# Kernel optimization log

Hardware: AMD Instinct MI355X
Metric: run time of the kernel (lower is better)

The kernel has to match this reference:

```python
import jax, jax.numpy as jnp
import numpy as np

NUM_HEADS = 16
HEAD_DIM = 80
DIM = NUM_HEADS * HEAD_DIM
SEQ = 2048
SCALE = HEAD_DIM ** -0.5


def rotate_half(x):
    x1, x2 = jnp.split(x, 2, axis=-1)
    return jnp.concatenate((-x2, x1), axis=-1)


def setup_inputs() -> dict:
    key = jax.random.key(0)
    ks = jax.random.split(key, 8)
    hidden_states = jax.random.normal(ks[0], (SEQ, DIM), dtype=jnp.float32)
    cu_seqlens = jnp.array([0, SEQ], dtype=jnp.int32)  # unused by the math
    # rotary embeddings for head_dim
    inv_freq = 1.0 / (10000.0 ** (jnp.arange(0, HEAD_DIM // 2, dtype=jnp.float32) / (HEAD_DIM // 2)))
    freqs = jnp.outer(jnp.arange(SEQ, dtype=jnp.float32), inv_freq)  # [S, hd/2]
    emb = jnp.concatenate((freqs, freqs), axis=-1)  # [S, hd]
    cos = jnp.cos(emb)
    sin = jnp.sin(emb)
    w_qkv = jax.random.normal(ks[1], (3 * DIM, DIM), dtype=jnp.float32) * (DIM ** -0.5)
    b_qkv = jax.random.normal(ks[2], (3 * DIM,), dtype=jnp.float32) * 0.02
    w_proj = jax.random.normal(ks[3], (DIM, DIM), dtype=jnp.float32) * (DIM ** -0.5)
    b_proj = jax.random.normal(ks[4], (DIM,), dtype=jnp.float32) * 0.02
    return {"hidden_states": hidden_states, "cu_seqlens": cu_seqlens, "cos": cos,
            "sin": sin, "w_qkv": w_qkv, "b_qkv": b_qkv, "w_proj": w_proj, "b_proj": b_proj}


def reference(hidden_states, cu_seqlens, cos, sin, w_qkv, b_qkv, w_proj, b_proj):
    S = hidden_states.shape[0]
    qkv = hidden_states @ w_qkv.T + b_qkv  # [S, 3*D]
    qkv = qkv.reshape(S, 3, NUM_HEADS, HEAD_DIM)
    q, k, v = qkv[:, 0], qkv[:, 1], qkv[:, 2]  # each [S, H, hd]
    c = cos[:, None, :]  # [S, 1, hd]
    s = sin[:, None, :]
    q = q * c + rotate_half(q) * s
    k = k * c + rotate_half(k) * s
    # SDPA, non-causal: [H, S, S]
    scores = jnp.einsum('shd,thd->hst', q, k) * SCALE
    attn = jax.nn.softmax(scores, axis=-1)
    out = jnp.einsum('hst,thd->shd', attn, v).reshape(S, DIM)
    return out @ w_proj.T + b_proj
```

## Files before the change

### kernel.cpp

```cpp
#include <hip/hip_runtime.h>


#define SEQLEN   2048
#define DIMM     1280
#define NHEADS   16
#define HD       80
#define HDP      96
#define QKV_N    3840
#define NSPLIT   4
#define KVSPAN   (SEQLEN / NSPLIT)
#define QSCALE_LOG2E 0.16130083587064776f

#define KSTRIDE  104
#define VSTRIDE  72

#define EXP2F(x) __builtin_amdgcn_exp2f(x)

#define GLD16(gptr, lptr)                                                      \
    __builtin_amdgcn_global_load_lds(                                          \
        (const __attribute__((address_space(1))) void*)(gptr),                 \
        (__attribute__((address_space(3))) void*)(lptr), 16, 0, 0)

typedef float f32x4 __attribute__((ext_vector_type(4)));
typedef _Float16 half8 __attribute__((ext_vector_type(8)));
typedef _Float16 half4 __attribute__((ext_vector_type(4)));

static __device__ __forceinline__ f32x4 mfma_16x16x32(half8 a, half8 b, f32x4 c) {
    return __builtin_amdgcn_mfma_f32_16x16x32_f16(a, b, c, 0, 0, 0);
}
static __device__ __forceinline__ f32x4 mfma_16x16x16(half4 a, half4 b, f32x4 c) {
    return __builtin_amdgcn_mfma_f32_16x16x16f16(a, b, c, 0, 0, 0);
}

__global__ __launch_bounds__(256)
void cast_all(const float* __restrict__ hs, const float* __restrict__ wq,
              const float* __restrict__ wp, _Float16* __restrict__ dhs,
              _Float16* __restrict__ dwq, _Float16* __restrict__ dwp) {
    const int n1 = SEQLEN * DIMM / 4, n2 = QKV_N * DIMM / 4, n3 = DIMM * DIMM / 4;
    int i = blockIdx.x * 256 + threadIdx.x;
    const float4* src; half4* dst; int j;
    if (i < n1)           { src = (const float4*)hs; dst = (half4*)dhs; j = i; }
    else if (i < n1 + n2) { src = (const float4*)wq; dst = (half4*)dwq; j = i - n1; }
    else if (i < n1 + n2 + n3) { src = (const float4*)wp; dst = (half4*)dwp; j = i - n1 - n2; }
    else return;
    const float4 v = src[j];
    half4 h;
    h.x = (_Float16)v.x; h.y = (_Float16)v.y;
    h.z = (_Float16)v.z; h.w = (_Float16)v.w;
    dst[j] = h;
}

template<bool OUT_F16>
__global__ __launch_bounds__(256, 2)
void gemm_bt(const _Float16* __restrict__ A, const _Float16* __restrict__ B,
             const float* __restrict__ bias, void* __restrict__ Cout,
             int M, int N, int K) {
    __shared__ __align__(16) _Float16 As[128 * 32];
    __shared__ __align__(16) _Float16 Bs[128 * 32];
    const int tid  = threadIdx.x;
    const int lane = tid & 63;
    const int wave = tid >> 6;
    const int l15  = lane & 15;
    const int quad = lane >> 4;
    const int wm   = wave & 1;
    const int wn   = wave >> 1;
    const long bm = blockIdx.x, bn = blockIdx.y;

    const _Float16* Ag = A + bm * 128 * (long)K;
    const _Float16* Bg = B + bn * 128 * (long)K;

    const int srow = lane >> 2;
    const int scol = (lane & 3) * 8;
    f32x4 acc[4][4] = {};

    for (int k0 = 0; k0 < K; k0 += 32) {
        __syncthreads();
#pragma unroll
        for (int cc = 0; cc < 2; cc++) {
            const int c = wave + cc * 4;
            const long row = 16 * c + srow;
            GLD16(Ag + row * K + k0 + scol, As + 512 * c + lane * 8);
            GLD16(Bg + row * K + k0 + scol, Bs + 512 * c + lane * 8);
        }
        __syncthreads();
        half8 af[4], bf[4];
#pragma unroll
        for (int t = 0; t < 4; t++) {
            af[t] = *(const half8*)&As[(wm * 64 + t * 16 + l15) * 32 + quad * 8];
            bf[t] = *(const half8*)&Bs[(wn * 64 + t * 16 + l15) * 32 + quad * 8];
        }
#pragma unroll
        for (int mt = 0; mt < 4; mt++)
#pragma unroll
            for (int nt = 0; nt < 4; nt++)
                acc[mt][nt] = mfma_16x16x32(af[mt], bf[nt], acc[mt][nt]);
    }

    float bv[4];
#pragma unroll
    for (int nt = 0; nt < 4; nt++)
        bv[nt] = bias[bn * 128 + wn * 64 + nt * 16 + l15];

#pragma unroll
    for (int mt = 0; mt < 4; mt++) {
#pragma unroll
        for (int r = 0; r < 4; r++) {
            const long row = bm * 128 + wm * 64 + mt * 16 + quad * 4 + r;
#pragma unroll
            for (int nt = 0; nt < 4; nt++) {
                const long col = bn * 128 + wn * 64 + nt * 16 + l15;
                const float v = acc[mt][nt][r] + bv[nt];
                if (OUT_F16) ((_Float16*)Cout)[row * (long)N + col] = (_Float16)v;
                else         ((float*)Cout)[row * (long)N + col] = v;
            }
        }
    }
}

__global__ __launch_bounds__(256)
void rope_repack(const _Float16* __restrict__ qkv,
                 const float* __restrict__ cosb,
                 const float* __restrict__ sinb,
                 _Float16* __restrict__ Qh,
                 _Float16* __restrict__ Kh,
                 _Float16* __restrict__ Vh) {
    const int s = blockIdx.x;
    const int tid = threadIdx.x;
    const _Float16* row = qkv + (long)s * QKV_N;

    for (int i = tid; i < NHEADS * 5; i += 256) {
        const int h = i / 5, d = (i - h * 5) * 8;
        const half8 q0 = *(const half8*)&row[h * HD + d];
        const half8 q1 = *(const half8*)&row[h * HD + d + 40];
        const half8 k0 = *(const half8*)&row[DIMM + h * HD + d];
        const half8 k1 = *(const half8*)&row[DIMM + h * HD + d + 40];
        const float4 cA = *(const float4*)&cosb[s * HD + d];
        const float4 cB = *(const float4*)&cosb[s * HD + d + 4];
        const float4 sA = *(const float4*)&sinb[s * HD + d];
        const float4 sB = *(const float4*)&sinb[s * HD + d + 4];
        half8 qo0, qo1, ko0, ko1;
#pragma unroll
        for (int j = 0; j < 8; j++) {
            const float cj = (j < 4) ? cA[j] : cB[j - 4];
            const float sj = (j < 4) ? sA[j] : sB[j - 4];
            qo0[j] = (_Float16)(((float)q0[j] * cj - (float)q1[j] * sj) * QSCALE_LOG2E);
            qo1[j] = (_Float16)(((float)q1[j] * cj + (float)q0[j] * sj) * QSCALE_LOG2E);
            ko0[j] = (_Float16)((float)k0[j] * cj - (float)k1[j] * sj);
            ko1[j] = (_Float16)((float)k1[j] * cj + (float)k0[j] * sj);
        }
        const long o = ((long)h * SEQLEN + s) * HDP;
        *(half8*)&Qh[o + d]      = qo0;
        *(half8*)&Qh[o + d + 40] = qo1;
        *(half8*)&Kh[o + d]      = ko0;
        *(half8*)&Kh[o + d + 40] = ko1;
    }
    for (int i = tid; i < NHEADS * 10; i += 256) {
        const int h = i / 10, d = (i - h * 10) * 8;
        *(half8*)&Vh[((long)h * SEQLEN + s) * HDP + d] =
            *(const half8*)&row[2 * DIMM + h * HD + d];
    }
    for (int i = tid; i < NHEADS * 2; i += 256) {
        const int h = i >> 1, d = HD + (i & 1) * 8;
        const long o = ((long)h * SEQLEN + s) * HDP + d;
        *(half8*)&Qh[o] = (half8)(_Float16)0.f;
        *(half8*)&Kh[o] = (half8)(_Float16)0.f;
    }
}

__global__ __launch_bounds__(256)
void v_transpose(const _Float16* __restrict__ Vh, _Float16* __restrict__ Vt) {
    const int s0 = blockIdx.x * 64;
    const int h  = blockIdx.y;
    __shared__ __align__(16) _Float16 Ts[64 * 88];
    const int tid = threadIdx.x;
    for (int i = tid; i < 640; i += 256) {
        const int r = i / 10, c = (i - r * 10) * 8;
        *(half8*)&Ts[r * 88 + c] =
            *(const half8*)&Vh[((long)h * SEQLEN + s0 + r) * HDP + c];
    }
    __syncthreads();
    for (int i = tid; i < 640; i += 256) {
        const int d = i >> 3, sc = (i & 7) * 8;
        half8 v;
#pragma unroll
        for (int j = 0; j < 8; j++) v[j] = Ts[(sc + j) * 88 + d];
        *(half8*)&Vt[((long)h * HD + d) * SEQLEN + s0 + sc] = v;
    }
}

__global__ __launch_bounds__(512, 8)
void attn_kernel(const _Float16* __restrict__ Qh, const _Float16* __restrict__ Kh,
                 const _Float16* __restrict__ Vt,
                 _Float16* __restrict__ Ohat0, _Float16* __restrict__ Ohat1,
                 float* __restrict__ Lpart) {
    const int s0 = blockIdx.x * 128;
    const int h  = blockIdx.y;
    const int z  = blockIdx.z;
    __shared__ __align__(16) _Float16 Ks[64 * KSTRIDE];
    __shared__ __align__(16) _Float16 Vts[HD * VSTRIDE];

    const int tid  = threadIdx.x;
    const int lane = tid & 63;
    const int wave = tid >> 6;
    const int l15  = lane & 15;
    const int quad = lane >> 4;

    const _Float16* Qg = Qh + ((long)h * SEQLEN + s0 + wave * 16 + l15) * HDP;
    half8 qf[3];
#pragma unroll
    for (int kk = 0; kk < 3; kk++)
        qf[kk] = *(const half8*)&Qg[kk * 32 + quad * 8];

    f32x4 oaccT[5] = {};
    float l_acc = 0.f;

    for (int t0 = z * KVSPAN; t0 < (z + 1) * KVSPAN; t0 += 64) {
        __syncthreads();
        const _Float16* Kg = Kh + ((long)h * SEQLEN + t0) * HDP;
        for (int i = tid; i < 768; i += 512) {
            const int r = i / 12, c = (i - r * 12) * 8;
            *(half8*)&Ks[r * KSTRIDE + c] = *(const half8*)&Kg[(long)r * HDP + c];
        }
        const _Float16* Vtg = Vt + (long)h * HD * SEQLEN + t0;
        for (int i = tid; i < 640; i += 512) {
            const int d = i >> 3, c = (i & 7) * 8;
            *(half8*)&Vts[d * VSTRIDE + c] = *(const half8*)&Vtg[(long)d * SEQLEN + c];
        }
        __syncthreads();

        f32x4 sa[4] = {};
#pragma unroll
        for (int kk = 0; kk < 3; kk++)
#pragma unroll
            for (int ct = 0; ct < 4; ct++) {
                half8 kf = *(const half8*)&Ks[(ct * 16 + l15) * KSTRIDE + kk * 32 + quad * 8];
                sa[ct] = mfma_16x16x32(kf, qf[kk], sa[ct]);
            }

        half4 pb[4];
#pragma unroll
        for (int ct = 0; ct < 4; ct++)
#pragma unroll
            for (int r = 0; r < 4; r++) {
                const float p = EXP2F(sa[ct][r]);
                l_acc += p;
                pb[ct][r] = (_Float16)p;
            }

#pragma unroll
        for (int nt = 0; nt < 5; nt++)
#pragma unroll
            for (int ct = 0; ct < 4; ct++) {
                half4 vf = *(const half4*)&Vts[(nt * 16 + l15) * VSTRIDE + ct * 16 + quad * 4];
                oaccT[nt] = mfma_16x16x16(vf, pb[ct], oaccT[nt]);
            }
    }

    l_acc += __shfl_xor(l_acc, 16);
    l_acc += __shfl_xor(l_acc, 32);
    const float inv = 1.0f / l_acc;

    _Float16* Oz = (z < 2) ? Ohat0 : Ohat1;
    const long obase = ((long)(z & 1) * NHEADS + h) * SEQLEN;
    const long lbase = ((long)z * NHEADS + h) * SEQLEN;
    const long row = s0 + wave * 16 + l15;
#pragma unroll
    for (int nt = 0; nt < 5; nt++) {
        half4 o;
#pragma unroll
        for (int r = 0; r < 4; r++) o[r] = (_Float16)(oaccT[nt][r] * inv);
        *(half4*)&Oz[(obase + row) * HD + nt * 16 + quad * 4] = o;
    }
    if (quad == 0)
        Lpart[lbase + row] = l_acc;
}

__global__ __launch_bounds__(256)
void attn_combine(const _Float16* __restrict__ Ohat0,
                  const _Float16* __restrict__ Ohat1,
                  const float* __restrict__ Lp,
                  _Float16* __restrict__ attnb) {
    const int i = blockIdx.x * 256 + threadIdx.x;
    if (i >= SEQLEN * DIMM / 4) return;
    const int flat = i * 4;
    const int s = flat / DIMM;
    const int rem = flat - s * DIMM;
    const int h = rem / HD;
    const int d = rem - h * HD;
    float l[NSPLIT], lsum = 0.f;
#pragma unroll
    for (int zi = 0; zi < NSPLIT; zi++) {
        l[zi] = Lp[((long)zi * NHEADS + h) * SEQLEN + s];
        lsum += l[zi];
    }
    const float invl = 1.0f / lsum;
    float acc[4] = {0.f, 0.f, 0.f, 0.f};
#pragma unroll
    for (int zi = 0; zi < NSPLIT; zi++) {
        const _Float16* Oz = (zi < 2) ? Ohat0 : Ohat1;
        const long obase = ((long)(zi & 1) * NHEADS + h) * SEQLEN;
        const half4 o = *(const half4*)&Oz[(obase + s) * HD + d];
        const float w = l[zi] * invl;
#pragma unroll
        for (int j = 0; j < 4; j++) acc[j] += (float)o[j] * w;
    }
    half4 o;
#pragma unroll
    for (int j = 0; j < 4; j++) o[j] = (_Float16)acc[j];
    *(half4*)&attnb[(long)s * DIMM + rem] = o;
}

extern "C" void kernel_launch(void* const* d_in, const int* in_sizes, int n_in,
                              void* d_out, int out_size, void* d_ws, size_t ws_size,
                              hipStream_t stream) {
    const float* hs     = (const float*)d_in[0];
    const float* cosb   = (const float*)d_in[2];
    const float* sinb   = (const float*)d_in[3];
    const float* w_qkv  = (const float*)d_in[4];
    const float* b_qkv  = (const float*)d_in[5];
    const float* w_proj = (const float*)d_in[6];
    const float* b_proj = (const float*)d_in[7];
    float* out = (float*)d_out;

    _Float16* hsb    = (_Float16*)d_ws;
    _Float16* wqkvb  = hsb    + (long)SEQLEN * DIMM;
    _Float16* wprojb = wqkvb  + (long)QKV_N * DIMM;
    _Float16* qkv    = wprojb + (long)DIMM * DIMM;
    _Float16* Qh     = qkv    + (long)SEQLEN * QKV_N;
    _Float16* Kh     = Qh     + (long)NHEADS * SEQLEN * HDP;
    _Float16* Vh     = Kh     + (long)NHEADS * SEQLEN * HDP;
    _Float16* Vtb    = Vh     + (long)NHEADS * SEQLEN * HDP;
    _Float16* attnb  = Vtb    + (long)NHEADS * HD * SEQLEN;

    _Float16* Ohat0  = (_Float16*)d_ws;
    float*    LpartB = (float*)(Ohat0 + (long)2 * NHEADS * SEQLEN * HD);
    _Float16* Ohat1  = qkv;

    {
        const int ntot = (SEQLEN * DIMM + QKV_N * DIMM + DIMM * DIMM) / 4;
        cast_all<<<(ntot + 255) / 256, 256, 0, stream>>>(
            hs, w_qkv, w_proj, hsb, wqkvb, wprojb);
    }

    gemm_bt<true><<<dim3(SEQLEN / 128, QKV_N / 128), 256, 0, stream>>>(
        hsb, wqkvb, b_qkv, qkv, SEQLEN, QKV_N, DIMM);

    rope_repack<<<SEQLEN, 256, 0, stream>>>(qkv, cosb, sinb, Qh, Kh, Vh);

    v_transpose<<<dim3(SEQLEN / 64, NHEADS), 256, 0, stream>>>(Vh, Vtb);

    attn_kernel<<<dim3(SEQLEN / 128, NHEADS, NSPLIT), 512, 0, stream>>>(
        Qh, Kh, Vtb, Ohat0, Ohat1, LpartB);

    attn_combine<<<(SEQLEN * DIMM / 4 + 255) / 256, 256, 0, stream>>>(
        Ohat0, Ohat1, LpartB, attnb);

    gemm_bt<false><<<dim3(SEQLEN / 128, DIMM / 128), 256, 0, stream>>>(
        attnb, wprojb, b_proj, out, SEQLEN, DIMM, DIMM);
}
```

Baseline: 219.2 us.

## Fuse RoPE with V transpose, pre-swizzle V in LDS, split-K output projection

Three changes land together. The RoPE repack and V transpose kernels merge into one per-(64 rows, head) kernel that writes transposed V straight from the qkv buffer, which drops the intermediate Vh buffer and one launch. The attention kernel now stores V in LDS in MFMA fragment order, so each lane reads two half8 vectors per tile instead of four half4 loads. The output projection uses split-K over two z-slices with atomic float adds into a memset output, doubling the block count for the small 16x10 grid. The cost is an extra memset, atomic traffic, and nondeterministic summation order.

```diff
diff --git a/kernel.cpp b/kernel.cpp
--- a/kernel.cpp
+++ b/kernel.cpp
@@ -12,7 +12,6 @@
 #define QSCALE_LOG2E 0.16130083587064776f
 
 #define KSTRIDE  104
-#define VSTRIDE  72
 
 #define EXP2F(x) __builtin_amdgcn_exp2f(x)
 
@@ -30,6 +29,12 @@
 }
 static __device__ __forceinline__ f32x4 mfma_16x16x16(half4 a, half4 b, f32x4 c) {
     return __builtin_amdgcn_mfma_f32_16x16x16f16(a, b, c, 0, 0, 0);
+}
+static __device__ __forceinline__ half4 lo4(half8 v) {
+    return __builtin_shufflevector(v, v, 0, 1, 2, 3);
+}
+static __device__ __forceinline__ half4 hi4(half8 v) {
+    return __builtin_shufflevector(v, v, 4, 5, 6, 7);
 }
 
 __global__ __launch_bounds__(256)
@@ -117,27 +122,101 @@
     }
 }
 
+__global__ __launch_bounds__(256, 2)
+void gemm_bt_sk(const _Float16* __restrict__ A, const _Float16* __restrict__ B,
+                const float* __restrict__ bias, float* __restrict__ Cout,
+                int M, int N, int K) {
+    __shared__ __align__(16) _Float16 As[128 * 32];
+    __shared__ __align__(16) _Float16 Bs[128 * 32];
+    const int tid  = threadIdx.x;
+    const int lane = tid & 63;
+    const int wave = tid >> 6;
+    const int l15  = lane & 15;
+    const int quad = lane >> 4;
+    const int wm   = wave & 1;
+    const int wn   = wave >> 1;
+    const long bm = blockIdx.x, bn = blockIdx.y;
+    const int  z  = blockIdx.z;
+    const int  kHalf = K / 2;
+
+    const _Float16* Ag = A + bm * 128 * (long)K;
+    const _Float16* Bg = B + bn * 128 * (long)K;
+
+    const int srow = lane >> 2;
+    const int scol = (lane & 3) * 8;
+    f32x4 acc[4][4] = {};
+
+    for (int k0 = z * kHalf; k0 < (z + 1) * kHalf; k0 += 32) {
+        __syncthreads();
+#pragma unroll
+        for (int cc = 0; cc < 2; cc++) {
+            const int c = wave + cc * 4;
+            const long row = 16 * c + srow;
+            GLD16(Ag + row * K + k0 + scol, As + 512 * c + lane * 8);
+            GLD16(Bg + row * K + k0 + scol, Bs + 512 * c + lane * 8);
+        }
+        __syncthreads();
+        half8 af[4], bf[4];
+#pragma unroll
+        for (int t = 0; t < 4; t++) {
+            af[t] = *(const half8*)&As[(wm * 64 + t * 16 + l15) * 32 + quad * 8];
+            bf[t] = *(const half8*)&Bs[(wn * 64 + t * 16 + l15) * 32 + quad * 8];
+        }
+#pragma unroll
+        for (int mt = 0; mt < 4; mt++)
+#pragma unroll
+            for (int nt = 0; nt < 4; nt++)
+                acc[mt][nt] = mfma_16x16x32(af[mt], bf[nt], acc[mt][nt]);
+    }
+
+    float bv[4];
+#pragma unroll
+    for (int nt = 0; nt < 4; nt++)
+        bv[nt] = (z == 0) ? bias[bn * 128 + wn * 64 + nt * 16 + l15] : 0.f;
+
+#pragma unroll
+    for (int mt = 0; mt < 4; mt++) {
+#pragma unroll
+        for (int r = 0; r < 4; r++) {
+            const long row = bm * 128 + wm * 64 + mt * 16 + quad * 4 + r;
+#pragma unroll
+            for (int nt = 0; nt < 4; nt++) {
+                const long col = bn * 128 + wn * 64 + nt * 16 + l15;
+                unsafeAtomicAdd(&Cout[row * (long)N + col], acc[mt][nt][r] + bv[nt]);
+            }
+        }
+    }
+}
+
 __global__ __launch_bounds__(256)
-void rope_repack(const _Float16* __restrict__ qkv,
-                 const float* __restrict__ cosb,
-                 const float* __restrict__ sinb,
-                 _Float16* __restrict__ Qh,
-                 _Float16* __restrict__ Kh,
-                 _Float16* __restrict__ Vh) {
-    const int s = blockIdx.x;
+void rope_repack_t(const _Float16* __restrict__ qkv,
+                   const float* __restrict__ cosb,
+                   const float* __restrict__ sinb,
+                   _Float16* __restrict__ Qh,
+                   _Float16* __restrict__ Kh,
+                   _Float16* __restrict__ Vt) {
+    const int s0 = blockIdx.x * 64;
+    const int h  = blockIdx.y;
+    __shared__ __align__(16) _Float16 Ts[64 * 88];
     const int tid = threadIdx.x;
-    const _Float16* row = qkv + (long)s * QKV_N;
-
-    for (int i = tid; i < NHEADS * 5; i += 256) {
-        const int h = i / 5, d = (i - h * 5) * 8;
-        const half8 q0 = *(const half8*)&row[h * HD + d];
-        const half8 q1 = *(const half8*)&row[h * HD + d + 40];
-        const half8 k0 = *(const half8*)&row[DIMM + h * HD + d];
-        const half8 k1 = *(const half8*)&row[DIMM + h * HD + d + 40];
-        const float4 cA = *(const float4*)&cosb[s * HD + d];
-        const float4 cB = *(const float4*)&cosb[s * HD + d + 4];
-        const float4 sA = *(const float4*)&sinb[s * HD + d];
-        const float4 sB = *(const float4*)&sinb[s * HD + d + 4];
+
+    for (int i = tid; i < 640; i += 256) {
+        const int r = i / 10, c = (i - r * 10) * 8;
+        *(half8*)&Ts[r * 88 + c] =
+            *(const half8*)&qkv[(long)(s0 + r) * QKV_N + 2 * DIMM + h * HD + c];
+    }
+
+    for (int i = tid; i < 320; i += 256) {
+        const int r = i / 5, d = (i - r * 5) * 8;
+        const _Float16* row = qkv + (long)(s0 + r) * QKV_N + h * HD;
+        const half8 q0 = *(const half8*)&row[d];
+        const half8 q1 = *(const half8*)&row[d + 40];
+        const half8 k0 = *(const half8*)&row[DIMM + d];
+        const half8 k1 = *(const half8*)&row[DIMM + d + 40];
+        const float4 cA = *(const float4*)&cosb[(s0 + r) * HD + d];
+        const float4 cB = *(const float4*)&cosb[(s0 + r) * HD + d + 4];
+        const float4 sA = *(const float4*)&sinb[(s0 + r) * HD + d];
+        const float4 sB = *(const float4*)&sinb[(s0 + r) * HD + d + 4];
         half8 qo0, qo1, ko0, ko1;
 #pragma unroll
         for (int j = 0; j < 8; j++) {
@@ -148,35 +227,17 @@
             ko0[j] = (_Float16)((float)k0[j] * cj - (float)k1[j] * sj);
             ko1[j] = (_Float16)((float)k1[j] * cj + (float)k0[j] * sj);
         }
-        const long o = ((long)h * SEQLEN + s) * HDP;
+        const long o = ((long)h * SEQLEN + s0 + r) * HDP;
         *(half8*)&Qh[o + d]      = qo0;
         *(half8*)&Qh[o + d + 40] = qo1;
         *(half8*)&Kh[o + d]      = ko0;
         *(half8*)&Kh[o + d + 40] = ko1;
     }
-    for (int i = tid; i < NHEADS * 10; i += 256) {
-        const int h = i / 10, d = (i - h * 10) * 8;
-        *(half8*)&Vh[((long)h * SEQLEN + s) * HDP + d] =
-            *(const half8*)&row[2 * DIMM + h * HD + d];
-    }
-    for (int i = tid; i < NHEADS * 2; i += 256) {
-        const int h = i >> 1, d = HD + (i & 1) * 8;
-        const long o = ((long)h * SEQLEN + s) * HDP + d;
+    for (int i = tid; i < 128; i += 256) {
+        const int r = i >> 1, off = HD + (i & 1) * 8;
+        const long o = ((long)h * SEQLEN + s0 + r) * HDP + off;
         *(half8*)&Qh[o] = (half8)(_Float16)0.f;
         *(half8*)&Kh[o] = (half8)(_Float16)0.f;
-    }
-}
-
-__global__ __launch_bounds__(256)
-void v_transpose(const _Float16* __restrict__ Vh, _Float16* __restrict__ Vt) {
-    const int s0 = blockIdx.x * 64;
-    const int h  = blockIdx.y;
-    __shared__ __align__(16) _Float16 Ts[64 * 88];
-    const int tid = threadIdx.x;
-    for (int i = tid; i < 640; i += 256) {
-        const int r = i / 10, c = (i - r * 10) * 8;
-        *(half8*)&Ts[r * 88 + c] =
-            *(const half8*)&Vh[((long)h * SEQLEN + s0 + r) * HDP + c];
     }
     __syncthreads();
     for (int i = tid; i < 640; i += 256) {
@@ -197,7 +258,7 @@
     const int h  = blockIdx.y;
     const int z  = blockIdx.z;
     __shared__ __align__(16) _Float16 Ks[64 * KSTRIDE];
-    __shared__ __align__(16) _Float16 Vts[HD * VSTRIDE];
+    __shared__ __align__(16) _Float16 VF[5 * 64 * 16];
 
     const int tid  = threadIdx.x;
     const int lane = tid & 63;
@@ -224,7 +285,11 @@
         const _Float16* Vtg = Vt + (long)h * HD * SEQLEN + t0;
         for (int i = tid; i < 640; i += 512) {
             const int d = i >> 3, c = (i & 7) * 8;
-            *(half8*)&Vts[d * VSTRIDE + c] = *(const half8*)&Vtg[(long)d * SEQLEN + c];
+            const half8 v = *(const half8*)&Vtg[(long)d * SEQLEN + c];
+            const int nt = d >> 4, ld = d & 15;
+            const int ct = c >> 4, qb = (c & 15) >> 2;
+            *(half4*)&VF[(nt * 64 + qb * 16 + ld) * 16 + ct * 4]       = lo4(v);
+            *(half4*)&VF[(nt * 64 + (qb + 1) * 16 + ld) * 16 + ct * 4] = hi4(v);
         }
         __syncthreads();
 
@@ -248,12 +313,14 @@
             }
 
 #pragma unroll
-        for (int nt = 0; nt < 5; nt++)
-#pragma unroll
-            for (int ct = 0; ct < 4; ct++) {
-                half4 vf = *(const half4*)&Vts[(nt * 16 + l15) * VSTRIDE + ct * 16 + quad * 4];
-                oaccT[nt] = mfma_16x16x16(vf, pb[ct], oaccT[nt]);
-            }
+        for (int nt = 0; nt < 5; nt++) {
+            const half8 va = *(const half8*)&VF[(nt * 64 + lane) * 16];
+            const half8 vb = *(const half8*)&VF[(nt * 64 + lane) * 16 + 8];
+            oaccT[nt] = mfma_16x16x16(lo4(va), pb[0], oaccT[nt]);
+            oaccT[nt] = mfma_16x16x16(hi4(va), pb[1], oaccT[nt]);
+            oaccT[nt] = mfma_16x16x16(lo4(vb), pb[2], oaccT[nt]);
+            oaccT[nt] = mfma_16x16x16(hi4(vb), pb[3], oaccT[nt]);
+        }
     }
 
     l_acc += __shfl_xor(l_acc, 16);
@@ -328,8 +395,7 @@
     _Float16* qkv    = wprojb + (long)DIMM * DIMM;
     _Float16* Qh     = qkv    + (long)SEQLEN * QKV_N;
     _Float16* Kh     = Qh     + (long)NHEADS * SEQLEN * HDP;
-    _Float16* Vh     = Kh     + (long)NHEADS * SEQLEN * HDP;
-    _Float16* Vtb    = Vh     + (long)NHEADS * SEQLEN * HDP;
+    _Float16* Vtb    = Kh     + (long)NHEADS * SEQLEN * HDP;
     _Float16* attnb  = Vtb    + (long)NHEADS * HD * SEQLEN;
 
     _Float16* Ohat0  = (_Float16*)d_ws;
@@ -345,9 +411,8 @@
     gemm_bt<true><<<dim3(SEQLEN / 128, QKV_N / 128), 256, 0, stream>>>(
         hsb, wqkvb, b_qkv, qkv, SEQLEN, QKV_N, DIMM);
 
-    rope_repack<<<SEQLEN, 256, 0, stream>>>(qkv, cosb, sinb, Qh, Kh, Vh);
-
-    v_transpose<<<dim3(SEQLEN / 64, NHEADS), 256, 0, stream>>>(Vh, Vtb);
+    rope_repack_t<<<dim3(SEQLEN / 64, NHEADS), 256, 0, stream>>>(
+        qkv, cosb, sinb, Qh, Kh, Vtb);
 
     attn_kernel<<<dim3(SEQLEN / 128, NHEADS, NSPLIT), 512, 0, stream>>>(
         Qh, Kh, Vtb, Ohat0, Ohat1, LpartB);
@@ -355,6 +420,7 @@
     attn_combine<<<(SEQLEN * DIMM / 4 + 255) / 256, 256, 0, stream>>>(
         Ohat0, Ohat1, LpartB, attnb);
 
-    gemm_bt<false><<<dim3(SEQLEN / 128, DIMM / 128), 256, 0, stream>>>(
+    hipMemsetAsync(out, 0, (size_t)SEQLEN * DIMM * sizeof(float), stream);
+    gemm_bt_sk<<<dim3(SEQLEN / 128, DIMM / 128, 2), 256, 0, stream>>>(
         attnb, wprojb, b_proj, out, SEQLEN, DIMM, DIMM);
 }
```

New measurement: 219.3 us. No clear change (+0.0%).
